# Performance work log

Hardware: AMD Instinct MI355X
Metric: run time of the kernel (lower is better)

Reference implementation:

```python
import jax, jax.numpy as jnp
import numpy as np

D_IN = 1024
D_OUT = 1024


def setup_inputs() -> dict:
    key = jax.random.key(0)
    kx, kq, kk, kv = jax.random.split(key, 4)
    B, T = 8, 2048
    x = jax.random.normal(kx, (B, T, D_IN), dtype=jnp.float32)
    # torch Linear weight is (d_out, d_in); we store transposed (d_in, d_out)
    s = 1.0 / np.sqrt(D_IN)
    Wq = jax.random.uniform(kq, (D_IN, D_OUT), jnp.float32, -s, s)
    Wk = jax.random.uniform(kk, (D_IN, D_OUT), jnp.float32, -s, s)
    Wv = jax.random.uniform(kv, (D_IN, D_OUT), jnp.float32, -s, s)
    return {"x": x, "Wq": Wq, "Wk": Wk, "Wv": Wv}


def reference(x, Wq, Wk, Wv):
    # x: (B, T, d_in)
    T = x.shape[1]
    d_out = Wq.shape[1]
    q = jnp.einsum('btd,de->bte', x, Wq)  # (B,T,d_out)
    k = jnp.einsum('btd,de->bte', x, Wk)
    v = jnp.einsum('btd,de->bte', x, Wv)
    scores = jnp.einsum('bqe,bke->bqk', q, k)  # (B,T,T)
    causal = jnp.tril(jnp.ones((T, T), dtype=bool))  # True = keep
    scores = jnp.where(causal[None], scores, -jnp.inf)
    weights = jax.nn.softmax(scores / jnp.sqrt(jnp.asarray(d_out, x.dtype)), axis=-1)
    # dropout p=0.0 -> identity
    return jnp.einsum('bqk,bke->bqe', weights, v)  # (B,T,d_out)
```

## Files before the change

### kernel.cpp

```cpp
#include <hip/hip_runtime.h>

using u16 = unsigned short;
typedef __bf16 bf16x8 __attribute__((ext_vector_type(8)));
typedef unsigned short u16x8 __attribute__((ext_vector_type(8)));
typedef float floatx4 __attribute__((ext_vector_type(4)));

__device__ __forceinline__ u16 f2bf(float f) {
  union { float f; unsigned u; } c; c.f = f;
  unsigned u = c.u;
  u += 0x7fffu + ((u >> 16) & 1u);
  return (u16)(u >> 16);
}
__device__ __forceinline__ float bf2f(u16 h) {
  union { unsigned u; float f; } c; c.u = ((unsigned)h) << 16; return c.f;
}

__device__ __forceinline__ void st_out(float* p, float v) { *p = v; }
__device__ __forceinline__ void st_out(u16* p, float v) { *p = f2bf(v); }

__device__ __forceinline__ void load16(const u16* g, u16* l) {
  __builtin_amdgcn_global_load_lds(
      (const __attribute__((address_space(1))) void*)g,
      (__attribute__((address_space(3))) void*)l, 16, 0, 0);
}

#define TILE 128
#define BK 64

template<typename OutT>
__device__ __forceinline__ void gemm_core(
    const u16* __restrict__ A, int lda, long sA,
    const u16* __restrict__ Bt, int ldb, long sB,
    OutT* __restrict__ C, int ldc, long sC,
    int kmax, int bx, int by, int bz, int tid)
{
  __shared__ u16 As[TILE * BK];
  __shared__ u16 Bs[TILE * BK];

  const u16* Ab = A + bz * sA + (long)by * TILE * lda;
  const u16* Bb = Bt + bz * sB + (long)bx * TILE * ldb;

  int lane = tid & 63;
  int wm = ((tid >> 7) & 1) * 64;
  int wn = ((tid >> 6) & 1) * 64;

  floatx4 acc[4][4] = {};
  int arow = wm + (lane & 15);
  int brow = wn + (lane & 15);
  int q = lane >> 4;

  for (int k0 = 0; k0 < kmax; k0 += BK) {
    __syncthreads();
#pragma unroll
    for (int h = 0; h < 4; h++) {
      int cc = tid + h * 256;
      int row = cc >> 3, gm = (cc & 7) ^ (row & 7);
      load16(Ab + (long)row * lda + k0 + gm * 8, &As[cc * 8]);
    }
#pragma unroll
    for (int h = 0; h < 4; h++) {
      int cc = tid + h * 256;
      int row = cc >> 3, gm = (cc & 7) ^ (row & 7);
      load16(Bb + (long)row * ldb + k0 + gm * 8, &Bs[cc * 8]);
    }
    __builtin_amdgcn_s_waitcnt(0);
    __syncthreads();

#pragma unroll
    for (int kp = 0; kp < 2; kp++) {
      bf16x8 a[4], b[4];
#pragma unroll
      for (int i = 0; i < 4; i++) {
        int r = arow + i * 16;
        a[i] = *(const bf16x8*)&As[(r * 8 + ((kp * 4 + q) ^ (r & 7))) * 8];
      }
#pragma unroll
      for (int j = 0; j < 4; j++) {
        int r = brow + j * 16;
        b[j] = *(const bf16x8*)&Bs[(r * 8 + ((kp * 4 + q) ^ (r & 7))) * 8];
      }
#pragma unroll
      for (int i = 0; i < 4; i++)
#pragma unroll
        for (int j = 0; j < 4; j++)
          acc[i][j] = __builtin_amdgcn_mfma_f32_16x16x32_bf16(a[i], b[j], acc[i][j], 0, 0, 0);
    }
  }

  OutT* Cb = C + bz * sC;
  int colbase = bx * TILE + wn + (lane & 15);
  int rowbase = by * TILE + wm + ((lane >> 4) << 2);
#pragma unroll
  for (int i = 0; i < 4; i++)
#pragma unroll
    for (int j = 0; j < 4; j++) {
      int col = colbase + j * 16;
#pragma unroll
      for (int r = 0; r < 4; r++)
        st_out(&Cb[(long)(rowbase + i * 16 + r) * ldc + col], acc[i][j][r]);
    }
}

template<typename OutT>
__global__ __launch_bounds__(256, 2)
void gemm_rect(const u16* __restrict__ A, int lda, long sA,
               const u16* __restrict__ Bt, int ldb, long sB,
               OutT* __restrict__ C, int ldc, long sC, int K,
               int l2gx, int nO8s)
{
  int L = blockIdx.x;
  int t = ((L & 7) << nO8s) | (L >> 3);
  int bx = t & ((1 << l2gx) - 1), by = t >> l2gx;
  gemm_core<OutT>(A, lda, sA, Bt, ldb, sB, C, ldc, sC, K, bx, by, blockIdx.y, threadIdx.x);
}

__global__ __launch_bounds__(256, 2)
void gemm_tri(const u16* __restrict__ A, int lda, long sA,
              const u16* __restrict__ Bt, int ldb, long sB,
              u16* __restrict__ C, int ldc, long sC, int K)
{
  int tp = blockIdx.x;
  int g = (tp & 7) * 17 + (tp >> 3);
  int sr = 0, sc = 0, pre = 0;
  for (;;) {
    int sz = (sr == sc) ? 3 : 4;
    if (pre + sz > g) break;
    pre += sz; ++sc;
    if (sc > sr) { ++sr; sc = 0; }
  }
  int w = g - pre;
  int r, c;
  if (sr == sc) { r = 2 * sr + (w > 0); c = 2 * sc + (w == 2); }
  else          { r = 2 * sr + (w >> 1); c = 2 * sc + (w & 1); }
  gemm_core<u16>(A, lda, sA, Bt, ldb, sB, C, ldc, sC, K, c, r, blockIdx.y, threadIdx.x);
}

__global__ __launch_bounds__(256, 2)
void gemm_opv(const u16* __restrict__ P, int lda, long sA,
              const u16* __restrict__ VT, int ldb, long sB,
              float* __restrict__ C, int ldc, long sC)
{
  int L = blockIdx.x;
  int j = L & 7, s = L >> 3;
  int by = (s < 8) ? 15 - j : j;
  int bx = s & 7;
  gemm_core<float>(P, lda, sA, VT, ldb, sB, C, ldc, sC,
                   (by + 1) * TILE, bx, by, blockIdx.y, threadIdx.x);
}

template<typename OutT>
__device__ __forceinline__ void gemm_core256(
    const u16* __restrict__ A, int lda, long sA,
    const u16* __restrict__ Bt, int ldb, long sB,
    OutT* __restrict__ C, int ldc, long sC,
    int kmax, int bx, int by, int bz, int tid, u16* lds)
{
  const u16* Ab = A + bz * sA + (long)by * 256 * lda;
  const u16* Bb = Bt + bz * sB + (long)bx * 256 * ldb;

  const int lane = tid & 63, wid = tid >> 6;
  const int wm = wid >> 2;
  const int wn = wid & 3;
  const int l15 = lane & 15, q = lane >> 4;

  const int cc0 = tid, cc1 = tid + 512;
  const int r0 = cc0 >> 3, g0 = (cc0 & 7) ^ (r0 & 7);
  const int r1 = cc1 >> 3, g1 = (cc1 & 7) ^ (r1 & 7);

  const int NK = kmax >> 6;

  floatx4 acc[8][4] = {};

  auto STAGE_A = [&](int k, int half, int buf) {
    const u16* g = Ab + (long)(half * 128) * lda + k * 64;
    load16(g + (long)r0 * lda + g0 * 8, lds + buf + half * 8192 + cc0 * 8);
    load16(g + (long)r1 * lda + g1 * 8, lds + buf + half * 8192 + cc1 * 8);
  };
  auto STAGE_B = [&](int k, int half, int buf) {
    const u16* g = Bb + (long)(half * 128) * ldb + k * 64;
    load16(g + (long)r0 * ldb + g0 * 8, lds + buf + 16384 + half * 8192 + cc0 * 8);
    load16(g + (long)r1 * ldb + g1 * 8, lds + buf + 16384 + half * 8192 + cc1 * 8);
  };

  STAGE_B(0, 0, 0); STAGE_B(0, 1, 0);
  STAGE_A(0, 0, 0); STAGE_A(0, 1, 0);
  if (NK > 1) {
    STAGE_B(1, 0, 32768); STAGE_B(1, 1, 32768);
    STAGE_A(1, 0, 32768);
    asm volatile("s_waitcnt vmcnt(6)" ::: "memory");
  } else {
    asm volatile("s_waitcnt vmcnt(0)" ::: "memory");
  }
  __builtin_amdgcn_s_barrier();

  const int s0 = (q ^ (l15 & 7)) * 8;
  const int s1 = ((q + 4) ^ (l15 & 7)) * 8;

  bf16x8 aL[2][4], aH[2][4], bL[2][2], bH[2][2];

  for (int t = 0; t < NK; ++t) {
    const int buf = (t & 1) ? 32768 : 0;
    const int nbuf = 32768 - buf;
    const int abase = buf + wm * 8192 + l15 * 64;
    const int bbase = buf + 16384 + (wn >> 1) * 8192 + ((wn & 1) * 64 + l15) * 64;

#pragma unroll
    for (int i = 0; i < 4; ++i) {
      aL[0][i] = *(const bf16x8*)&lds[abase + i * 1024 + s0];
      aL[1][i] = *(const bf16x8*)&lds[abase + i * 1024 + s1];
    }
#pragma unroll
    for (int j = 0; j < 2; ++j) {
      bL[0][j] = *(const bf16x8*)&lds[bbase + j * 1024 + s0];
      bL[1][j] = *(const bf16x8*)&lds[bbase + j * 1024 + s1];
    }
    if (t + 1 < NK) STAGE_A(t + 1, 1, nbuf);
    asm volatile("s_waitcnt lgkmcnt(8)" ::: "memory");
    __builtin_amdgcn_s_barrier();
    asm volatile("s_waitcnt lgkmcnt(0)" ::: "memory");
    __builtin_amdgcn_s_setprio(1);
#pragma unroll
    for (int kp = 0; kp < 2; ++kp)
#pragma unroll
      for (int i = 0; i < 4; ++i)
#pragma unroll
        for (int j = 0; j < 2; ++j)
          acc[i][j] = __builtin_amdgcn_mfma_f32_16x16x32_bf16(aL[kp][i], bL[kp][j], acc[i][j], 0, 0, 0);
    __builtin_amdgcn_s_setprio(0);
    asm volatile("" ::: "memory");
    __builtin_amdgcn_s_barrier();

#pragma unroll
    for (int j = 0; j < 2; ++j) {
      bH[0][j] = *(const bf16x8*)&lds[bbase + (2 + j) * 1024 + s0];
      bH[1][j] = *(const bf16x8*)&lds[bbase + (2 + j) * 1024 + s1];
    }
    asm volatile("" ::: "memory");
    __builtin_amdgcn_s_barrier();
    asm volatile("s_waitcnt lgkmcnt(0)" ::: "memory");
    __builtin_amdgcn_s_setprio(1);
#pragma unroll
    for (int kp = 0; kp < 2; ++kp)
#pragma unroll
      for (int i = 0; i < 4; ++i)
#pragma unroll
        for (int j = 0; j < 2; ++j)
          acc[i][2 + j] = __builtin_amdgcn_mfma_f32_16x16x32_bf16(aL[kp][i], bH[kp][j], acc[i][2 + j], 0, 0, 0);
    __builtin_amdgcn_s_setprio(0);
    asm volatile("" ::: "memory");
    __builtin_amdgcn_s_barrier();

#pragma unroll
    for (int i = 0; i < 4; ++i) {
      aH[0][i] = *(const bf16x8*)&lds[abase + 4096 + i * 1024 + s0];
      aH[1][i] = *(const bf16x8*)&lds[abase + 4096 + i * 1024 + s1];
    }
    if (t + 2 < NK) { STAGE_B(t + 2, 0, buf); STAGE_B(t + 2, 1, buf); }
    asm volatile("" ::: "memory");
    __builtin_amdgcn_s_barrier();
    asm volatile("s_waitcnt lgkmcnt(0)" ::: "memory");
    __builtin_amdgcn_s_setprio(1);
#pragma unroll
    for (int kp = 0; kp < 2; ++kp)
#pragma unroll
      for (int i = 0; i < 4; ++i)
#pragma unroll
        for (int j = 0; j < 2; ++j)
          acc[4 + i][2 + j] = __builtin_amdgcn_mfma_f32_16x16x32_bf16(aH[kp][i], bH[kp][j], acc[4 + i][2 + j], 0, 0, 0);
    __builtin_amdgcn_s_setprio(0);
    asm volatile("" ::: "memory");
    __builtin_amdgcn_s_barrier();

    if (t + 2 < NK) {
      STAGE_A(t + 2, 0, buf);
      asm volatile("s_waitcnt vmcnt(6)" ::: "memory");
    } else {
      asm volatile("s_waitcnt vmcnt(0)" ::: "memory");
    }
    __builtin_amdgcn_s_barrier();
    __builtin_amdgcn_s_setprio(1);
#pragma unroll
    for (int kp = 0; kp < 2; ++kp)
#pragma unroll
      for (int i = 0; i < 4; ++i)
#pragma unroll
        for (int j = 0; j < 2; ++j)
          acc[4 + i][j] = __builtin_amdgcn_mfma_f32_16x16x32_bf16(aH[kp][i], bL[kp][j], acc[4 + i][j], 0, 0, 0);
    __builtin_amdgcn_s_setprio(0);
    asm volatile("" ::: "memory");
    __builtin_amdgcn_s_barrier();
  }

  OutT* Cb = C + bz * sC;
  const int colbase = bx * 256 + wn * 64 + l15;
  const int rowbase = by * 256 + wm * 128 + (q << 2);
#pragma unroll
  for (int i = 0; i < 8; ++i)
#pragma unroll
    for (int j = 0; j < 4; ++j) {
      const int col = colbase + j * 16;
#pragma unroll
      for (int r = 0; r < 4; ++r)
        st_out(&Cb[(long)(rowbase + i * 16 + r) * ldc + col], acc[i][j][r]);
    }
}

__global__ __launch_bounds__(512, 2)
void gemm256_y(const u16* __restrict__ xb, const u16* __restrict__ NT,
               u16* __restrict__ Yb)
{
  extern __shared__ u16 lds[];
  int L = blockIdx.x;
  int t = ((L & 7) << 5) | (L >> 3);
  int bx = t & 3, by = t >> 2;
  gemm_core256<u16>(xb, 1024, 0L, NT, 1024, 0L, Yb, 1024, 0L,
                    1024, bx, by, 0, (int)threadIdx.x, lds);
}

__global__ __launch_bounds__(512, 2)
void gemm256_vt(const u16* __restrict__ WvT, const u16* __restrict__ xb,
                u16* __restrict__ VT)
{
  extern __shared__ u16 lds[];
  int L = blockIdx.x;
  int t = ((L & 7) << 5) | (L >> 3);
  int bx = t & 63, by = t >> 6;
  gemm_core256<u16>(WvT, 1024, 0L, xb, 1024, 0L, VT, 16384, 0L,
                    1024, bx, by, 0, (int)threadIdx.x, lds);
}

__global__ __launch_bounds__(256)
void cvt_in(const float4* __restrict__ x, const float4* __restrict__ Wq,
            const float4* __restrict__ Wk, u16* __restrict__ xb,
            u16* __restrict__ oq, u16* __restrict__ ok, int n4x, int n4w)
{
  int i = blockIdx.x * 256 + threadIdx.x;
  const float4* src; u16* dst; int k; float scale;
  if (i < n4x)               { src = x;  dst = xb; k = i;            scale = 1.0f; }
  else if (i < n4x + n4w)    { src = Wq; dst = oq; k = i - n4x;      scale = 0.03125f; }
  else if (i < n4x + 2*n4w)  { src = Wk; dst = ok; k = i - n4x - n4w; scale = 1.0f; }
  else return;
  float4 v = src[k];
  ushort4 r;
  r.x = f2bf(v.x * scale); r.y = f2bf(v.y * scale);
  r.z = f2bf(v.z * scale); r.w = f2bf(v.w * scale);
  *(ushort4*)(dst + (long)k * 4) = r;
}

__global__ __launch_bounds__(256)
void cvt_w(const float* __restrict__ W, u16* __restrict__ O)
{
  const int D = 1024;
  __shared__ float t[64][65];
  int tid = threadIdx.x;
  int c = tid & 63, r = tid >> 6;
  int e0 = blockIdx.x * 64, d0 = blockIdx.y * 64;
  for (int rr = r; rr < 64; rr += 4)
    t[rr][c] = W[(long)(d0 + rr) * D + e0 + c];
  __syncthreads();
  for (int rr = r; rr < 64; rr += 4)
    O[(long)(e0 + rr) * D + d0 + c] = f2bf(t[c][rr]);
}

__global__ __launch_bounds__(256)
void softmax_bf16(u16* __restrict__ S)
{
  const int T = 2048;
  int row = blockIdx.x & (T - 1);
  u16* Prow = S + (long)blockIdx.x * T;
  int n = row + 1;
  int W = ((row >> 7) + 1) << 7;
  int tid = threadIdx.x, lane = tid & 63, wid = tid >> 6;
  int i0 = tid * 8;
  bool act = (i0 < W);

  float v[8];
  float lmax = -3.0e38f;
  if (act) {
    u16x8 pv = *(const u16x8*)(Prow + i0);
#pragma unroll
    for (int j = 0; j < 8; j++) {
      v[j] = (i0 + j < n) ? bf2f(pv[j]) : -3.0e38f;
      lmax = fmaxf(lmax, v[j]);
    }
  }
  __shared__ float red[8];
#pragma unroll
  for (int o = 32; o > 0; o >>= 1) lmax = fmaxf(lmax, __shfl_down(lmax, o, 64));
  if (lane == 0) red[wid] = lmax;
  __syncthreads();
  float m = fmaxf(fmaxf(red[0], red[1]), fmaxf(red[2], red[3]));

  float lsum = 0.f;
  if (act) {
#pragma unroll
    for (int j = 0; j < 8; j++) {
      float e = (i0 + j < n) ? __expf(v[j] - m) : 0.f;
      v[j] = e;
      lsum += e;
    }
  }
#pragma unroll
  for (int o = 32; o > 0; o >>= 1) lsum += __shfl_down(lsum, o, 64);
  if (lane == 0) red[4 + wid] = lsum;
  __syncthreads();
  float inv = 1.0f / (red[4] + red[5] + red[6] + red[7]);

  if (act) {
    u16x8 w;
#pragma unroll
    for (int j = 0; j < 8; j++) w[j] = f2bf(v[j] * inv);
    *(u16x8*)(Prow + i0) = w;
  }
}

extern "C" void kernel_launch(void* const* d_in, const int* in_sizes, int n_in,
                              void* d_out, int out_size, void* d_ws, size_t ws_size,
                              hipStream_t stream)
{
  const int B = 8, T = 2048, D = 1024;
  const float* x  = (const float*)d_in[0];
  const float* Wq = (const float*)d_in[1];
  const float* Wk = (const float*)d_in[2];
  const float* Wv = (const float*)d_in[3];
  float* out = (float*)d_out;
  char* ws = (char*)d_ws;

  u16* xb  = (u16*)(ws);
  u16* WvT = (u16*)(ws + (32ul << 20));
  u16* NT  = (u16*)(ws + (34ul << 20));
  u16* Yb  = (u16*)(ws + (36ul << 20));
  u16* Wqb = Yb;
  u16* Wkb = (u16*)(ws + (38ul << 20));
  u16* VT  = (u16*)(ws + (68ul << 20));
  u16* S   = (u16*)(ws + (100ul << 20));

  const size_t OFF_S = 100ul << 20;
  int NB = 8;
  while (NB > 1 && OFF_S + (size_t)NB * T * T * 2 > ws_size) NB >>= 1;

  static bool attr_done = false;
  if (!attr_done) {
    hipFuncSetAttribute(reinterpret_cast<const void*>(gemm256_y),
                        hipFuncAttributeMaxDynamicSharedMemorySize, 131072);
    hipFuncSetAttribute(reinterpret_cast<const void*>(gemm256_vt),
                        hipFuncAttributeMaxDynamicSharedMemorySize, 131072);
    attr_done = true;
  }

  int n4x = B * T * D / 4, n4w = D * D / 4;
  cvt_in<<<(n4x + 2 * n4w + 255) / 256, 256, 0, stream>>>(
      (const float4*)x, (const float4*)Wq, (const float4*)Wk,
      xb, Wqb, Wkb, n4x, n4w);
  cvt_w<<<dim3(16, 16), 256, 0, stream>>>(Wv, WvT);

  gemm_rect<u16><<<dim3(64, 1), 256, 0, stream>>>(
      Wkb, D, 0L, Wqb, D, 0L, NT, D, 0L, D, 3, 3);
  gemm256_y<<<dim3(256, 1), 512, 131072, stream>>>(xb, NT, Yb);
  gemm256_vt<<<dim3(256, 1), 512, 131072, stream>>>(WvT, xb, VT);

  for (int b0 = 0; b0 < B; b0 += NB) {
    gemm_tri<<<dim3(136, NB), 256, 0, stream>>>(
        Yb + (long)b0 * T * D, D, (long)T * D,
        xb + (long)b0 * T * D, D, (long)T * D,
        S, T, (long)T * T, D);
    softmax_bf16<<<NB * T, 256, 0, stream>>>(S);
    gemm_opv<<<dim3(128, NB), 256, 0, stream>>>(
        S, T, (long)T * T,
        VT + (long)b0 * T, B * T, (long)T,
        out + (long)b0 * T * D, D, (long)T * D);
  }
}
```

Baseline: 367.0 us.

## Double-buffer 128-tile GEMM and merge Y and V projections into one launch

Adds a second LDS buffer to the 128x128 GEMM core so the next K-slice is fetched while the current one is consumed, dropping the per-iteration waitcnt and leading barrier. The two 256-tile projection GEMMs are fused into a single 512-block launch, removing one kernel launch and letting both halves share the device. VT changes from a (D, B*T) layout to per-batch (D, T) blocks, and the P·V consumer's strides are updated to match. The new prefetch has no explicit wait for its global-to-LDS loads before the barrier, so it relies on __syncthreads to cover outstanding load_lds ops, which risks a race. Doubling static LDS may also lower occupancy for the kernels that use this core.

```diff
diff --git a/kernel.cpp b/kernel.cpp
--- a/kernel.cpp
+++ b/kernel.cpp
@@ -34,8 +34,8 @@
     OutT* __restrict__ C, int ldc, long sC,
     int kmax, int bx, int by, int bz, int tid)
 {
-  __shared__ u16 As[TILE * BK];
-  __shared__ u16 Bs[TILE * BK];
+  __shared__ u16 As[2 * TILE * BK];
+  __shared__ u16 Bs[2 * TILE * BK];
 
   const u16* Ab = A + bz * sA + (long)by * TILE * lda;
   const u16* Bb = Bt + bz * sB + (long)bx * TILE * ldb;
@@ -49,35 +49,42 @@
   int brow = wn + (lane & 15);
   int q = lane >> 4;
 
-  for (int k0 = 0; k0 < kmax; k0 += BK) {
-    __syncthreads();
+  auto STAGE = [&](int k0, int buf) {
 #pragma unroll
     for (int h = 0; h < 4; h++) {
       int cc = tid + h * 256;
       int row = cc >> 3, gm = (cc & 7) ^ (row & 7);
-      load16(Ab + (long)row * lda + k0 + gm * 8, &As[cc * 8]);
+      load16(Ab + (long)row * lda + k0 + gm * 8, &As[buf * (TILE * BK) + cc * 8]);
     }
 #pragma unroll
     for (int h = 0; h < 4; h++) {
       int cc = tid + h * 256;
       int row = cc >> 3, gm = (cc & 7) ^ (row & 7);
-      load16(Bb + (long)row * ldb + k0 + gm * 8, &Bs[cc * 8]);
-    }
-    __builtin_amdgcn_s_waitcnt(0);
-    __syncthreads();
-
+      load16(Bb + (long)row * ldb + k0 + gm * 8, &Bs[buf * (TILE * BK) + cc * 8]);
+    }
+  };
+
+  STAGE(0, 0);
+  __syncthreads();
+
+  const int NK = kmax / BK;
+  for (int k = 0; k < NK; ++k) {
+    int cur = k & 1;
+    if (k + 1 < NK) STAGE((k + 1) * BK, cur ^ 1);
+
+    int cb = cur * (TILE * BK);
 #pragma unroll
     for (int kp = 0; kp < 2; kp++) {
       bf16x8 a[4], b[4];
 #pragma unroll
       for (int i = 0; i < 4; i++) {
         int r = arow + i * 16;
-        a[i] = *(const bf16x8*)&As[(r * 8 + ((kp * 4 + q) ^ (r & 7))) * 8];
+        a[i] = *(const bf16x8*)&As[cb + (r * 8 + ((kp * 4 + q) ^ (r & 7))) * 8];
       }
 #pragma unroll
       for (int j = 0; j < 4; j++) {
         int r = brow + j * 16;
-        b[j] = *(const bf16x8*)&Bs[(r * 8 + ((kp * 4 + q) ^ (r & 7))) * 8];
+        b[j] = *(const bf16x8*)&Bs[cb + (r * 8 + ((kp * 4 + q) ^ (r & 7))) * 8];
       }
 #pragma unroll
       for (int i = 0; i < 4; i++)
@@ -85,6 +92,7 @@
         for (int j = 0; j < 4; j++)
           acc[i][j] = __builtin_amdgcn_mfma_f32_16x16x32_bf16(a[i], b[j], acc[i][j], 0, 0, 0);
     }
+    __syncthreads();
   }
 
   OutT* Cb = C + bz * sC;
@@ -306,27 +314,26 @@
 }
 
 __global__ __launch_bounds__(512, 2)
-void gemm256_y(const u16* __restrict__ xb, const u16* __restrict__ NT,
-               u16* __restrict__ Yb)
+void gemm256_proj(const u16* __restrict__ xb, const u16* __restrict__ NT,
+                  const u16* __restrict__ WvT, u16* __restrict__ Yb,
+                  u16* __restrict__ VT)
 {
   extern __shared__ u16 lds[];
+  const int T = 2048, D = 1024;
   int L = blockIdx.x;
-  int t = ((L & 7) << 5) | (L >> 3);
-  int bx = t & 3, by = t >> 2;
-  gemm_core256<u16>(xb, 1024, 0L, NT, 1024, 0L, Yb, 1024, 0L,
-                    1024, bx, by, 0, (int)threadIdx.x, lds);
-}
-
-__global__ __launch_bounds__(512, 2)
-void gemm256_vt(const u16* __restrict__ WvT, const u16* __restrict__ xb,
-                u16* __restrict__ VT)
-{
-  extern __shared__ u16 lds[];
-  int L = blockIdx.x;
-  int t = ((L & 7) << 5) | (L >> 3);
-  int bx = t & 63, by = t >> 6;
-  gemm_core256<u16>(WvT, 1024, 0L, xb, 1024, 0L, VT, 16384, 0L,
-                    1024, bx, by, 0, (int)threadIdx.x, lds);
+  int t = ((L & 7) << 6) | (L >> 3);
+  if (t < 256) {
+    int bx = t & 3, by = t >> 2;
+    gemm_core256<u16>(xb, 1024, 0L, NT, 1024, 0L, Yb, 1024, 0L,
+                      1024, bx, by, 0, (int)threadIdx.x, lds);
+  } else {
+    int tt = t - 256;
+    int bt = tt & 63, by = tt >> 6;
+    int b = bt >> 3, bx = bt & 7;
+    gemm_core256<u16>(WvT, 1024, 0L, xb + (long)b * T * D, 1024, 0L,
+                      VT + (long)b * D * T, 2048, 0L,
+                      1024, bx, by, 0, (int)threadIdx.x, lds);
+  }
 }
 
 __global__ __launch_bounds__(256)
@@ -441,9 +448,7 @@
 
   static bool attr_done = false;
   if (!attr_done) {
-    hipFuncSetAttribute(reinterpret_cast<const void*>(gemm256_y),
-                        hipFuncAttributeMaxDynamicSharedMemorySize, 131072);
-    hipFuncSetAttribute(reinterpret_cast<const void*>(gemm256_vt),
+    hipFuncSetAttribute(reinterpret_cast<const void*>(gemm256_proj),
                         hipFuncAttributeMaxDynamicSharedMemorySize, 131072);
     attr_done = true;
   }
@@ -456,8 +461,7 @@
 
   gemm_rect<u16><<<dim3(64, 1), 256, 0, stream>>>(
       Wkb, D, 0L, Wqb, D, 0L, NT, D, 0L, D, 3, 3);
-  gemm256_y<<<dim3(256, 1), 512, 131072, stream>>>(xb, NT, Yb);
-  gemm256_vt<<<dim3(256, 1), 512, 131072, stream>>>(WvT, xb, VT);
+  gemm256_proj<<<dim3(512, 1), 512, 131072, stream>>>(xb, NT, WvT, Yb, VT);
 
   for (int b0 = 0; b0 < B; b0 += NB) {
     gemm_tri<<<dim3(136, NB), 256, 0, stream>>>(
@@ -467,7 +471,7 @@
     softmax_bf16<<<NB * T, 256, 0, stream>>>(S);
     gemm_opv<<<dim3(128, NB), 256, 0, stream>>>(
         S, T, (long)T * T,
-        VT + (long)b0 * T, B * T, (long)T,
+        VT + (long)b0 * D * T, 2048, (long)D * T,
         out + (long)b0 * T * D, D, (long)T * D);
   }
 }
```

Result: no change. 362.7 us (-1.2%).
